# Optimization experiments

Hardware: AMD Instinct MI355X
Metric: run time of the kernel (lower is better)

## Reference

```python
import jax, jax.numpy as jnp
import numpy as np

B, T, V, E, H, L = 16, 64, 50257, 512, 1024, 2


def _gru_layer(x, h0, W_ih, W_hh, b_ih, b_hh):
    # x: (T, B, I), h0: (B, H). PyTorch GRU gate order: r, z, n.
    xp = jnp.einsum('tbi,gi->tbg', x, W_ih) + b_ih  # precompute input gates (T, B, 3H)

    def step(h, xt):
        gh = h @ W_hh.T + b_hh
        xr, xz, xn = jnp.split(xt, 3, axis=-1)
        hr, hz, hn = jnp.split(gh, 3, axis=-1)
        r = jax.nn.sigmoid(xr + hr)
        z = jax.nn.sigmoid(xz + hz)
        n = jnp.tanh(xn + r * hn)
        h_new = (1.0 - z) * n + z * h
        return h_new, h_new

    hT, ys = jax.lax.scan(step, h0, xp)
    return ys, hT


def _gru(x, h0, layer_params):
    # h0: (L, B, H); stacked 2-layer GRU (dropout=0)
    hs = []
    for l in range(L):
        x, hl = _gru_layer(x, h0[l], *layer_params[l])
        hs.append(hl)
    return x, jnp.stack(hs)


def setup_inputs() -> dict:
    key = jax.random.key(0)
    ks = jax.random.split(key, 16)
    s = 0.03  # weight init scale
    return {
        'init_input': jax.random.normal(ks[0], (B, E), jnp.float32),
        'helper': jax.random.randint(ks[1], (B, T), 0, V),
        'emb': jax.random.normal(ks[2], (V, E), jnp.float32) * 0.1,
        'W_ih0': jax.random.normal(ks[3], (3 * H, 2 * E), jnp.float32) * s,
        'W_hh0': jax.random.normal(ks[4], (3 * H, H), jnp.float32) * s,
        'b_ih0': jax.random.normal(ks[5], (3 * H,), jnp.float32) * s,
        'b_hh0': jax.random.normal(ks[6], (3 * H,), jnp.float32) * s,
        'W_ih1': jax.random.normal(ks[7], (3 * H, H), jnp.float32) * s,
        'W_hh1': jax.random.normal(ks[8], (3 * H, H), jnp.float32) * s,
        'b_ih1': jax.random.normal(ks[9], (3 * H,), jnp.float32) * s,
        'b_hh1': jax.random.normal(ks[10], (3 * H,), jnp.float32) * s,
        'Wc_w': jax.random.normal(ks[11], (E, H), jnp.float32) * s,
        'Wc_b': jax.random.normal(ks[12], (E,), jnp.float32) * s,
    }


def reference(init_input, helper, emb, W_ih0, W_hh0, b_ih0, b_hh0,
              W_ih1, W_hh1, b_ih1, b_hh1, Wc_w, Wc_b):
    params = [(W_ih0, W_hh0, b_ih0, b_hh0), (W_ih1, W_hh1, b_ih1, b_hh1)]
    # h_0 from one GRU step over cat([init_input, init_input]) with zero state
    x0 = jnp.concatenate([init_input, init_input], axis=-1)[None]  # (1, B, 2E)
    h_zero = jnp.zeros((L, B, H), init_input.dtype)
    _, h0 = _gru(x0, h_zero, params)
    # teacher-forcing decode: helper embeddings concat with cond (init_input)
    helper_emb = emb[helper].transpose(1, 0, 2)  # (T, B, E)
    cond = jnp.broadcast_to(init_input[None], (T, B, E))
    x = jnp.concatenate([helper_emb, cond], axis=-1)  # (T, B, 2E)
    outputs, _ = _gru(x, h0, params)  # (T, B, H)
    final = jnp.tanh(jnp.einsum('tbh,eh->tbe', outputs, Wc_w) + Wc_b)  # (T, B, E)
    # dot-product word-embedding attention -> vocab logits, then transpose(0,1)
    logits = jnp.einsum('tbe,ve->btv', final, emb)  # (B, T, V)
    return logits
```

## Files before the change

### kernel.cpp

```cpp
#include <hip/hip_runtime.h>
#include <math.h>

#define Bc 16
#define Tc 64
#define Vc 50257
#define Ec 512
#define Hc 1024
#define SCAN_BLOCKS 256

typedef __attribute__((ext_vector_type(4))) float f32x4;
typedef __attribute__((ext_vector_type(8))) __bf16 bf16x8;

__device__ __forceinline__ float dot4(float4 a, float4 b) {
    return a.x * b.x + a.y * b.y + a.z * b.z + a.w * b.w;
}
__device__ __forceinline__ float sigm(float x) { return 1.0f / (1.0f + expf(-x)); }

__device__ __forceinline__ unsigned short f2b(float f) {
    unsigned u = __float_as_uint(f);
    unsigned r = u + 0x7fffu + ((u >> 16) & 1u);
    return (unsigned short)(r >> 16);
}
__device__ __forceinline__ float b2f(unsigned short b) {
    return __uint_as_float(((unsigned)b) << 16);
}
__device__ __forceinline__ float2 u2f2(unsigned long long u) {
    union { unsigned long long u; float2 f; } c;
    c.u = u;
    return c.f;
}
__device__ __forceinline__ unsigned long long f22u(float a, float b) {
    union { float f[2]; unsigned long long u; } c;
    c.f[0] = a;
    c.f[1] = b;
    return c.u;
}

__global__ __launch_bounds__(256) void split_bf16_4(const float4* __restrict__ x,
                                                    ushort4* __restrict__ hi,
                                                    ushort4* __restrict__ lo, int n4) {
    int i = blockIdx.x * 256 + threadIdx.x;
    for (; i < n4; i += gridDim.x * 256) {
        float4 v = x[i];
        ushort4 h, l;
        h.x = f2b(v.x); l.x = f2b(v.x - b2f(h.x));
        h.y = f2b(v.y); l.y = f2b(v.y - b2f(h.y));
        h.z = f2b(v.z); l.z = f2b(v.z - b2f(h.z));
        h.w = f2b(v.w); l.w = f2b(v.w - b2f(h.w));
        hi[i] = h;
        lo[i] = l;
    }
}

__global__ __launch_bounds__(256) void build_x0(const float* __restrict__ emb,
                                                const int* __restrict__ helper,
                                                const float* __restrict__ init,
                                                float* __restrict__ X0) {
    int idx = blockIdx.x * 256 + threadIdx.x;
    const int total = Tc * Bc * 1024;
    for (int i = idx; i < total; i += gridDim.x * 256) {
        int m = i >> 10;
        int c = i & 1023;
        int t = m >> 4;
        int b = m & 15;
        float v;
        if (c < 512) {
            int w = helper[b * Tc + t];
            v = emb[(size_t)w * Ec + c];
        } else {
            v = init[b * Ec + (c - 512)];
        }
        X0[i] = v;
    }
}

__global__ __launch_bounds__(256) void h0_layer(const float* __restrict__ xin,
                                                const float* __restrict__ Wih,
                                                const float* __restrict__ bih,
                                                const float* __restrict__ bhh,
                                                float* __restrict__ h0out, int dup) {
    __shared__ float xs[1024];
    int b = blockIdx.x >> 2;
    int hseg = blockIdx.x & 3;
    int tid = threadIdx.x;
    for (int i = tid; i < 1024; i += 256)
        xs[i] = dup ? xin[b * 512 + (i & 511)] : xin[b * 1024 + i];
    __syncthreads();
    int hidx = hseg * 256 + tid;
    const float* wr = Wih + (size_t)hidx * 1024;
    const float* wz = Wih + (size_t)(Hc + hidx) * 1024;
    const float* wn = Wih + (size_t)(2 * Hc + hidx) * 1024;
    float ar = 0.f, az = 0.f, an = 0.f;
    for (int k = 0; k < 1024; k += 4) {
        float4 x4 = *(const float4*)&xs[k];
        ar += dot4(*(const float4*)&wr[k], x4);
        az += dot4(*(const float4*)&wz[k], x4);
        an += dot4(*(const float4*)&wn[k], x4);
    }
    float r = sigm(ar + bih[hidx] + bhh[hidx]);
    float z = sigm(az + bih[Hc + hidx] + bhh[Hc + hidx]);
    float n = tanhf(an + bih[2 * Hc + hidx] + r * bhh[2 * Hc + hidx]);
    h0out[b * Hc + hidx] = (1.f - z) * n;
}

__global__ __launch_bounds__(512) void gru_scan(const float* __restrict__ xp,
                                                const float* __restrict__ Whh,
                                                const float* __restrict__ bhh,
                                                float* __restrict__ ys,
                                                unsigned* __restrict__ bar) {
    extern __shared__ char lds_pad[];
    __shared__ float wlds[12][1024];
    int tid = threadIdx.x;
    int g0 = blockIdx.x * 4;

    for (int i = tid; i < 12 * 256; i += 512) {
        int r = i >> 8, c = i & 255;
        int hl = r / 3, gate = r % 3;
        ((float4*)wlds[r])[c] =
            ((const float4*)&Whh[(size_t)(gate * Hc + g0 + hl) * Hc])[c];
    }

    int b = tid >> 5;
    int kseg = tid & 31;

    float bh[12];
    float hold[4];
    if (kseg == 0) {
#pragma unroll
        for (int r = 0; r < 12; ++r) {
            int hl = r / 3, gate = r % 3;
            bh[r] = bhh[gate * Hc + g0 + hl];
        }
        float4 h4 = *(const float4*)&ys[b * Hc + g0];
        hold[0] = h4.x; hold[1] = h4.y; hold[2] = h4.z; hold[3] = h4.w;
    }
    __syncthreads();

    unsigned* leaf = bar + (blockIdx.x & 15) * 32;
    unsigned* root = bar + 512;

    for (int t = 0; t < Tc; ++t) {
        float xg[3][4];
        if (kseg == 0) {
            const float* xrow = xp + (size_t)(t * Bc + b) * 3072 + g0;
#pragma unroll
            for (int gte = 0; gte < 3; ++gte) {
                float4 v = *(const float4*)&xrow[gte * 1024];
                xg[gte][0] = v.x; xg[gte][1] = v.y; xg[gte][2] = v.z; xg[gte][3] = v.w;
            }
        }
        const unsigned long long* hsrc =
            (const unsigned long long*)(ys + (size_t)t * (Bc * Hc)) + b * 512 + kseg;
        float2 hv[16];
#pragma unroll
        for (int q = 0; q < 16; ++q)
            hv[q] = u2f2(__hip_atomic_load(hsrc + q * 32, __ATOMIC_RELAXED,
                                           __HIP_MEMORY_SCOPE_AGENT));
        float acc[12];
#pragma unroll
        for (int r = 0; r < 12; ++r) {
            const float2* w = (const float2*)&wlds[r][kseg * 2];
            float s = 0.f;
#pragma unroll
            for (int q = 0; q < 16; ++q) {
                float2 ww = w[q * 32];
                s += ww.x * hv[q].x + ww.y * hv[q].y;
            }
            acc[r] = s;
        }
#pragma unroll
        for (int r = 0; r < 12; ++r) {
            float s = acc[r];
            s += __shfl_xor(s, 1);
            s += __shfl_xor(s, 2);
            s += __shfl_xor(s, 4);
            s += __shfl_xor(s, 8);
            s += __shfl_xor(s, 16);
            acc[r] = s;
        }
        if (kseg == 0) {
            float hnew[4];
#pragma unroll
            for (int hl = 0; hl < 4; ++hl) {
                float r_ = sigm(xg[0][hl] + acc[hl * 3 + 0] + bh[hl * 3 + 0]);
                float z_ = sigm(xg[1][hl] + acc[hl * 3 + 1] + bh[hl * 3 + 1]);
                float n_ = tanhf(xg[2][hl] + r_ * (acc[hl * 3 + 2] + bh[hl * 3 + 2]));
                hnew[hl] = (1.f - z_) * n_ + z_ * hold[hl];
                hold[hl] = hnew[hl];
            }
            unsigned long long* dst =
                (unsigned long long*)(ys + (size_t)(t + 1) * (Bc * Hc) + b * Hc + g0);
            __hip_atomic_store(dst, f22u(hnew[0], hnew[1]), __ATOMIC_RELAXED,
                               __HIP_MEMORY_SCOPE_AGENT);
            __hip_atomic_store(dst + 1, f22u(hnew[2], hnew[3]), __ATOMIC_RELAXED,
                               __HIP_MEMORY_SCOPE_AGENT);
        }
        if (t < Tc - 1) {
            __syncthreads();
            if (tid == 0) {
                unsigned old = __hip_atomic_fetch_add(leaf, 1u, __ATOMIC_RELAXED,
                                                      __HIP_MEMORY_SCOPE_AGENT);
                if (old == (unsigned)(t * 16 + 15))
                    __hip_atomic_fetch_add(root, 1u, __ATOMIC_RELAXED,
                                           __HIP_MEMORY_SCOPE_AGENT);
                unsigned tgt = (unsigned)((t + 1) * 16);
                while (__hip_atomic_load(root, __ATOMIC_RELAXED,
                                         __HIP_MEMORY_SCOPE_AGENT) < tgt)
                    __builtin_amdgcn_s_sleep(1);
            }
            __syncthreads();
        }
    }
}

#define GLD_LDS16(g, l)                                                        \
    __builtin_amdgcn_global_load_lds(                                          \
        (const __attribute__((address_space(1))) unsigned int*)(g),            \
        (__attribute__((address_space(3))) unsigned int*)(l), 16, 0, 0)

__global__ __launch_bounds__(256) void mfma_gemm_split(
    const unsigned short* __restrict__ Ah, const unsigned short* __restrict__ Al,
    const unsigned short* __restrict__ Bh, const unsigned short* __restrict__ Bl,
    const float* __restrict__ bias, float* __restrict__ C, int N, int K, int ldc,
    int act, int remap) {
    __shared__ __align__(16) unsigned short As[128 * 32];
    __shared__ __align__(16) unsigned short Bs[128 * 32];
    int tid = threadIdx.x;
    int m0 = blockIdx.y * 128, n0 = blockIdx.x * 128;
    int wave = tid >> 6, lane = tid & 63;
    int mh = (wave >> 1) * 64, nh = (wave & 1) * 64;
    int rlane = lane & 15, k8 = (lane >> 4) * 8;

    f32x4 zero = {0.f, 0.f, 0.f, 0.f};
    f32x4 acc[4][4];
#pragma unroll
    for (int i = 0; i < 4; ++i)
#pragma unroll
        for (int j = 0; j < 4; ++j) acc[i][j] = zero;

    const unsigned short* Ap[3] = {Ah, Al, Ah};
    const unsigned short* Bp[3] = {Bh, Bh, Bl};

    int c0 = tid, c1 = tid + 256;
    int ar0 = m0 + (c0 >> 2), ak0 = (c0 & 3) * 8;
    int ar1 = m0 + (c1 >> 2), ak1 = (c1 & 3) * 8;
    int br0 = n0 + (c0 >> 2);
    int br1 = n0 + (c1 >> 2);
    if (br0 >= N) br0 = N - 1;
    if (br1 >= N) br1 = N - 1;

    for (int ph = 0; ph < 3; ++ph) {
        const unsigned short* Ab = Ap[ph];
        const unsigned short* Bb = Bp[ph];
        for (int kt = 0; kt < K; kt += 32) {
            GLD_LDS16(&Ab[(size_t)ar0 * K + kt + ak0], &As[c0 * 8]);
            GLD_LDS16(&Ab[(size_t)ar1 * K + kt + ak1], &As[c1 * 8]);
            GLD_LDS16(&Bb[(size_t)br0 * K + kt + ak0], &Bs[c0 * 8]);
            GLD_LDS16(&Bb[(size_t)br1 * K + kt + ak1], &Bs[c1 * 8]);
            __syncthreads();
            bf16x8 a[4], b[4];
#pragma unroll
            for (int f = 0; f < 4; ++f)
                a[f] = *(const bf16x8*)&As[(mh + f * 16 + rlane) * 32 + k8];
#pragma unroll
            for (int f = 0; f < 4; ++f)
                b[f] = *(const bf16x8*)&Bs[(nh + f * 16 + rlane) * 32 + k8];
#pragma unroll
            for (int mf = 0; mf < 4; ++mf)
#pragma unroll
                for (int nf = 0; nf < 4; ++nf)
                    acc[mf][nf] = __builtin_amdgcn_mfma_f32_16x16x32_bf16(
                        a[mf], b[nf], acc[mf][nf], 0, 0, 0);
            __syncthreads();
        }
    }

    int quad = lane >> 4;
#pragma unroll
    for (int nf = 0; nf < 4; ++nf) {
        int n = n0 + nh + nf * 16 + rlane;
        if (n >= N) continue;
        float bv = bias ? bias[n] : 0.f;
#pragma unroll
        for (int mf = 0; mf < 4; ++mf) {
#pragma unroll
            for (int r = 0; r < 4; ++r) {
                int m = m0 + mh + mf * 16 + quad * 4 + r;
                float x = acc[mf][nf][r] + bv;
                if (act) x = tanhf(x);
                int orow = remap ? ((m & 15) * Tc + (m >> 4)) : m;
                C[(size_t)orow * ldc + n] = x;
            }
        }
    }
}

extern "C" void kernel_launch(void* const* d_in, const int* in_sizes, int n_in,
                              void* d_out, int out_size, void* d_ws, size_t ws_size,
                              hipStream_t stream) {
    const float* init   = (const float*)d_in[0];
    const int*   helper = (const int*)d_in[1];
    const float* emb    = (const float*)d_in[2];
    const float* W_ih0  = (const float*)d_in[3];
    const float* W_hh0  = (const float*)d_in[4];
    const float* b_ih0  = (const float*)d_in[5];
    const float* b_hh0  = (const float*)d_in[6];
    const float* W_ih1  = (const float*)d_in[7];
    const float* W_hh1  = (const float*)d_in[8];
    const float* b_ih1  = (const float*)d_in[9];
    const float* b_hh1  = (const float*)d_in[10];
    const float* Wc_w   = (const float*)d_in[11];
    const float* Wc_b   = (const float*)d_in[12];
    float* out = (float*)d_out;

    const int embN = Vc * Ec;

    char* p = (char*)d_ws;
    auto alloc = [&](size_t bytes) {
        char* r = p;
        p += (bytes + 255) & ~(size_t)255;
        return r;
    };
    float* X0   = (float*)alloc((size_t)1048576 * 4);
    float* xp0  = (float*)alloc((size_t)3145728 * 4);
    float* xp1  = (float*)alloc((size_t)3145728 * 4);
    float* ys0x = (float*)alloc((size_t)65 * 16384 * 4);
    float* ys1x = (float*)alloc((size_t)65 * 16384 * 4);
    float* fin  = (float*)alloc((size_t)524288 * 4);
    unsigned* bar = (unsigned*)alloc(8192);
    unsigned short* embh = (unsigned short*)alloc((size_t)embN * 2);
    unsigned short* embl = (unsigned short*)alloc((size_t)embN * 2);
    unsigned short* X0h  = (unsigned short*)alloc((size_t)1048576 * 2);
    unsigned short* X0l  = (unsigned short*)alloc((size_t)1048576 * 2);
    unsigned short* Wi0h = (unsigned short*)alloc((size_t)3145728 * 2);
    unsigned short* Wi0l = (unsigned short*)alloc((size_t)3145728 * 2);
    unsigned short* Wi1h = (unsigned short*)alloc((size_t)3145728 * 2);
    unsigned short* Wi1l = (unsigned short*)alloc((size_t)3145728 * 2);
    unsigned short* Wch  = (unsigned short*)alloc((size_t)524288 * 2);
    unsigned short* Wcl  = (unsigned short*)alloc((size_t)524288 * 2);
    unsigned short* ys0h = (unsigned short*)alloc((size_t)1048576 * 2);
    unsigned short* ys0l = (unsigned short*)alloc((size_t)1048576 * 2);
    unsigned short* ys1h = (unsigned short*)alloc((size_t)1048576 * 2);
    unsigned short* ys1l = (unsigned short*)alloc((size_t)1048576 * 2);
    unsigned short* finh = (unsigned short*)alloc((size_t)524288 * 2);
    unsigned short* finl = (unsigned short*)alloc((size_t)524288 * 2);

    hipMemsetAsync(bar, 0, 8192, stream);

    auto split = [&](const float* src, unsigned short* h, unsigned short* l, int n) {
        int n4 = n / 4;
        int grid = (n4 + 255) / 256;
        if (grid > 4096) grid = 4096;
        split_bf16_4<<<grid, 256, 0, stream>>>((const float4*)src, (ushort4*)h,
                                               (ushort4*)l, n4);
    };

    split(emb, embh, embl, embN);
    split(W_ih0, Wi0h, Wi0l, 3145728);
    split(W_ih1, Wi1h, Wi1l, 3145728);
    split(Wc_w, Wch, Wcl, 524288);

    h0_layer<<<64, 256, 0, stream>>>(init, W_ih0, b_ih0, b_hh0, ys0x, 1);
    h0_layer<<<64, 256, 0, stream>>>(ys0x, W_ih1, b_ih1, b_hh1, ys1x, 0);

    build_x0<<<1024, 256, 0, stream>>>(emb, helper, init, X0);
    split(X0, X0h, X0l, 1048576);
    mfma_gemm_split<<<dim3(24, 8), 256, 0, stream>>>(X0h, X0l, Wi0h, Wi0l, b_ih0,
                                                     xp0, 3072, 1024, 3072, 0, 0);
    gru_scan<<<SCAN_BLOCKS, 512, 40960, stream>>>(xp0, W_hh0, b_hh0, ys0x, bar);

    split(ys0x + 16384, ys0h, ys0l, 1048576);
    mfma_gemm_split<<<dim3(24, 8), 256, 0, stream>>>(ys0h, ys0l, Wi1h, Wi1l, b_ih1,
                                                     xp1, 3072, 1024, 3072, 0, 0);
    gru_scan<<<SCAN_BLOCKS, 512, 40960, stream>>>(xp1, W_hh1, b_hh1, ys1x, bar + 1024);

    split(ys1x + 16384, ys1h, ys1l, 1048576);
    mfma_gemm_split<<<dim3(4, 8), 256, 0, stream>>>(ys1h, ys1l, Wch, Wcl, Wc_b,
                                                    fin, 512, 1024, 512, 1, 0);

    split(fin, finh, finl, 524288);
    mfma_gemm_split<<<dim3((Vc + 127) / 128, 8), 256, 0, stream>>>(
        finh, finl, embh, embl, nullptr, out, Vc, 512, Vc, 0, 1);
}
```

Baseline: 2.258 ms.

## Wavefront-pipeline both GRU layers in one persistent scan kernel

Merges the two per-layer GRU scan kernels into one persistent kernel that runs layer 1 one step behind layer 0 (a wavefront over t=0..T). Layer 1's input projection is computed inside the scan from LDS-resident W_ih1 instead of a separate split + MFMA GEMM. This removes one kernel launch, one grid-wide barrier sequence of 64 steps, and the intermediate GEMM and split. The cost is 48K extra LDS plus a heavier per-step fp32 dot-product load per block, and W_ih1 is now applied in plain fp32 rather than through the split-bf16 MFMA path.

```diff
diff --git a/kernel.cpp b/kernel.cpp
--- a/kernel.cpp
+++ b/kernel.cpp
@@ -103,99 +103,195 @@
     h0out[b * Hc + hidx] = (1.f - z) * n;
 }
 
-__global__ __launch_bounds__(512) void gru_scan(const float* __restrict__ xp,
-                                                const float* __restrict__ Whh,
-                                                const float* __restrict__ bhh,
-                                                float* __restrict__ ys,
-                                                unsigned* __restrict__ bar) {
-    extern __shared__ char lds_pad[];
-    __shared__ float wlds[12][1024];
+__global__ __launch_bounds__(512) void gru_scan2(
+    const float* __restrict__ xp0, const float* __restrict__ Whh0,
+    const float* __restrict__ bhh0, const float* __restrict__ Wih1,
+    const float* __restrict__ Whh1, const float* __restrict__ bih1,
+    const float* __restrict__ bhh1, float* __restrict__ ys0,
+    float* __restrict__ ys1, unsigned* __restrict__ bar) {
+    extern __shared__ float wdyn[];
+    __shared__ float wh0[12][1024];
+    float* wi1 = wdyn;
+    float* wh1 = wdyn + 12 * 1024;
     int tid = threadIdx.x;
     int g0 = blockIdx.x * 4;
 
     for (int i = tid; i < 12 * 256; i += 512) {
         int r = i >> 8, c = i & 255;
         int hl = r / 3, gate = r % 3;
-        ((float4*)wlds[r])[c] =
-            ((const float4*)&Whh[(size_t)(gate * Hc + g0 + hl) * Hc])[c];
+        size_t row = (size_t)(gate * Hc + g0 + hl) * Hc;
+        ((float4*)wh0[r])[c] = ((const float4*)&Whh0[row])[c];
+        ((float4*)&wi1[r * 1024])[c] = ((const float4*)&Wih1[row])[c];
+        ((float4*)&wh1[r * 1024])[c] = ((const float4*)&Whh1[row])[c];
     }
 
     int b = tid >> 5;
     int kseg = tid & 31;
 
-    float bh[12];
-    float hold[4];
+    float bh0[12], brz1[8], bnx1[4], bnh1[4];
+    float hold0[4], hold1[4];
     if (kseg == 0) {
 #pragma unroll
         for (int r = 0; r < 12; ++r) {
             int hl = r / 3, gate = r % 3;
-            bh[r] = bhh[gate * Hc + g0 + hl];
-        }
-        float4 h4 = *(const float4*)&ys[b * Hc + g0];
-        hold[0] = h4.x; hold[1] = h4.y; hold[2] = h4.z; hold[3] = h4.w;
+            bh0[r] = bhh0[gate * Hc + g0 + hl];
+        }
+#pragma unroll
+        for (int hl = 0; hl < 4; ++hl) {
+            brz1[hl * 2 + 0] = bih1[g0 + hl] + bhh1[g0 + hl];
+            brz1[hl * 2 + 1] = bih1[Hc + g0 + hl] + bhh1[Hc + g0 + hl];
+            bnx1[hl] = bih1[2 * Hc + g0 + hl];
+            bnh1[hl] = bhh1[2 * Hc + g0 + hl];
+        }
+        float4 h4 = *(const float4*)&ys0[b * Hc + g0];
+        hold0[0] = h4.x; hold0[1] = h4.y; hold0[2] = h4.z; hold0[3] = h4.w;
+        float4 h5 = *(const float4*)&ys1[b * Hc + g0];
+        hold1[0] = h5.x; hold1[1] = h5.y; hold1[2] = h5.z; hold1[3] = h5.w;
     }
     __syncthreads();
 
     unsigned* leaf = bar + (blockIdx.x & 15) * 32;
     unsigned* root = bar + 512;
 
-    for (int t = 0; t < Tc; ++t) {
+    for (int t = 0; t <= Tc; ++t) {
+        const bool doL0 = (t < Tc);
+        const bool doL1 = (t > 0);
+
         float xg[3][4];
+        if (doL0 && kseg == 0) {
+            const float* xrow = xp0 + (size_t)(t * Bc + b) * 3072 + g0;
+#pragma unroll
+            for (int g = 0; g < 3; ++g) {
+                float4 v = *(const float4*)&xrow[g * 1024];
+                xg[g][0] = v.x; xg[g][1] = v.y; xg[g][2] = v.z; xg[g][3] = v.w;
+            }
+        }
+
+        const unsigned long long* h0src =
+            (const unsigned long long*)(ys0 + (size_t)t * (Bc * Hc)) + b * 512 + kseg;
+        float2 hv0[16];
+#pragma unroll
+        for (int q = 0; q < 16; ++q)
+            hv0[q] = u2f2(__hip_atomic_load(h0src + q * 32, __ATOMIC_RELAXED,
+                                            __HIP_MEMORY_SCOPE_AGENT));
+        float2 hv1[16];
+        if (doL1) {
+            const unsigned long long* h1src =
+                (const unsigned long long*)(ys1 + (size_t)(t - 1) * (Bc * Hc)) +
+                b * 512 + kseg;
+#pragma unroll
+            for (int q = 0; q < 16; ++q)
+                hv1[q] = u2f2(__hip_atomic_load(h1src + q * 32, __ATOMIC_RELAXED,
+                                                __HIP_MEMORY_SCOPE_AGENT));
+        }
+
+        float acc0[12];
+        if (doL0) {
+#pragma unroll
+            for (int r = 0; r < 12; ++r) {
+                const float2* w = (const float2*)&wh0[r][kseg * 2];
+                float s = 0.f;
+#pragma unroll
+                for (int q = 0; q < 16; ++q) {
+                    float2 ww = w[q * 32];
+                    s += ww.x * hv0[q].x + ww.y * hv0[q].y;
+                }
+                acc0[r] = s;
+            }
+        }
+
+        float a1[16];
+        if (doL1) {
+#pragma unroll
+            for (int hl = 0; hl < 4; ++hl) {
+#pragma unroll
+                for (int gate = 0; gate < 3; ++gate) {
+                    int r = hl * 3 + gate;
+                    const float2* wx = (const float2*)&wi1[r * 1024 + kseg * 2];
+                    const float2* wh = (const float2*)&wh1[r * 1024 + kseg * 2];
+                    float sx = 0.f, sh = 0.f;
+#pragma unroll
+                    for (int q = 0; q < 16; ++q) {
+                        float2 wwx = wx[q * 32];
+                        sx += wwx.x * hv0[q].x + wwx.y * hv0[q].y;
+                        float2 wwh = wh[q * 32];
+                        sh += wwh.x * hv1[q].x + wwh.y * hv1[q].y;
+                    }
+                    if (gate < 2)
+                        a1[hl * 4 + gate] = sx + sh;
+                    else {
+                        a1[hl * 4 + 2] = sx;
+                        a1[hl * 4 + 3] = sh;
+                    }
+                }
+            }
+        }
+
+        if (doL0) {
+#pragma unroll
+            for (int r = 0; r < 12; ++r) {
+                float s = acc0[r];
+                s += __shfl_xor(s, 1);
+                s += __shfl_xor(s, 2);
+                s += __shfl_xor(s, 4);
+                s += __shfl_xor(s, 8);
+                s += __shfl_xor(s, 16);
+                acc0[r] = s;
+            }
+        }
+        if (doL1) {
+#pragma unroll
+            for (int i = 0; i < 16; ++i) {
+                float s = a1[i];
+                s += __shfl_xor(s, 1);
+                s += __shfl_xor(s, 2);
+                s += __shfl_xor(s, 4);
+                s += __shfl_xor(s, 8);
+                s += __shfl_xor(s, 16);
+                a1[i] = s;
+            }
+        }
+
         if (kseg == 0) {
-            const float* xrow = xp + (size_t)(t * Bc + b) * 3072 + g0;
-#pragma unroll
-            for (int gte = 0; gte < 3; ++gte) {
-                float4 v = *(const float4*)&xrow[gte * 1024];
-                xg[gte][0] = v.x; xg[gte][1] = v.y; xg[gte][2] = v.z; xg[gte][3] = v.w;
-            }
-        }
-        const unsigned long long* hsrc =
-            (const unsigned long long*)(ys + (size_t)t * (Bc * Hc)) + b * 512 + kseg;
-        float2 hv[16];
-#pragma unroll
-        for (int q = 0; q < 16; ++q)
-            hv[q] = u2f2(__hip_atomic_load(hsrc + q * 32, __ATOMIC_RELAXED,
-                                           __HIP_MEMORY_SCOPE_AGENT));
-        float acc[12];
-#pragma unroll
-        for (int r = 0; r < 12; ++r) {
-            const float2* w = (const float2*)&wlds[r][kseg * 2];
-            float s = 0.f;
-#pragma unroll
-            for (int q = 0; q < 16; ++q) {
-                float2 ww = w[q * 32];
-                s += ww.x * hv[q].x + ww.y * hv[q].y;
-            }
-            acc[r] = s;
-        }
-#pragma unroll
-        for (int r = 0; r < 12; ++r) {
-            float s = acc[r];
-            s += __shfl_xor(s, 1);
-            s += __shfl_xor(s, 2);
-            s += __shfl_xor(s, 4);
-            s += __shfl_xor(s, 8);
-            s += __shfl_xor(s, 16);
-            acc[r] = s;
-        }
-        if (kseg == 0) {
-            float hnew[4];
-#pragma unroll
-            for (int hl = 0; hl < 4; ++hl) {
-                float r_ = sigm(xg[0][hl] + acc[hl * 3 + 0] + bh[hl * 3 + 0]);
-                float z_ = sigm(xg[1][hl] + acc[hl * 3 + 1] + bh[hl * 3 + 1]);
-                float n_ = tanhf(xg[2][hl] + r_ * (acc[hl * 3 + 2] + bh[hl * 3 + 2]));
-                hnew[hl] = (1.f - z_) * n_ + z_ * hold[hl];
-                hold[hl] = hnew[hl];
-            }
-            unsigned long long* dst =
-                (unsigned long long*)(ys + (size_t)(t + 1) * (Bc * Hc) + b * Hc + g0);
-            __hip_atomic_store(dst, f22u(hnew[0], hnew[1]), __ATOMIC_RELAXED,
-                               __HIP_MEMORY_SCOPE_AGENT);
-            __hip_atomic_store(dst + 1, f22u(hnew[2], hnew[3]), __ATOMIC_RELAXED,
-                               __HIP_MEMORY_SCOPE_AGENT);
-        }
-        if (t < Tc - 1) {
+            if (doL0) {
+                float hnew[4];
+#pragma unroll
+                for (int hl = 0; hl < 4; ++hl) {
+                    float r_ = sigm(xg[0][hl] + acc0[hl * 3 + 0] + bh0[hl * 3 + 0]);
+                    float z_ = sigm(xg[1][hl] + acc0[hl * 3 + 1] + bh0[hl * 3 + 1]);
+                    float n_ =
+                        tanhf(xg[2][hl] + r_ * (acc0[hl * 3 + 2] + bh0[hl * 3 + 2]));
+                    hnew[hl] = (1.f - z_) * n_ + z_ * hold0[hl];
+                    hold0[hl] = hnew[hl];
+                }
+                unsigned long long* dst = (unsigned long long*)(ys0 +
+                    (size_t)(t + 1) * (Bc * Hc) + b * Hc + g0);
+                __hip_atomic_store(dst, f22u(hnew[0], hnew[1]), __ATOMIC_RELAXED,
+                                   __HIP_MEMORY_SCOPE_AGENT);
+                __hip_atomic_store(dst + 1, f22u(hnew[2], hnew[3]), __ATOMIC_RELAXED,
+                                   __HIP_MEMORY_SCOPE_AGENT);
+            }
+            if (doL1) {
+                float hnew[4];
+#pragma unroll
+                for (int hl = 0; hl < 4; ++hl) {
+                    float r_ = sigm(a1[hl * 4 + 0] + brz1[hl * 2 + 0]);
+                    float z_ = sigm(a1[hl * 4 + 1] + brz1[hl * 2 + 1]);
+                    float n_ = tanhf(a1[hl * 4 + 2] + bnx1[hl] +
+                                     r_ * (a1[hl * 4 + 3] + bnh1[hl]));
+                    hnew[hl] = (1.f - z_) * n_ + z_ * hold1[hl];
+                    hold1[hl] = hnew[hl];
+                }
+                unsigned long long* dst = (unsigned long long*)(ys1 +
+                    (size_t)t * (Bc * Hc) + b * Hc + g0);
+                __hip_atomic_store(dst, f22u(hnew[0], hnew[1]), __ATOMIC_RELAXED,
+                                   __HIP_MEMORY_SCOPE_AGENT);
+                __hip_atomic_store(dst + 1, f22u(hnew[2], hnew[3]), __ATOMIC_RELAXED,
+                                   __HIP_MEMORY_SCOPE_AGENT);
+            }
+        }
+
+        if (t < Tc) {
             __syncthreads();
             if (tid == 0) {
                 unsigned old = __hip_atomic_fetch_add(leaf, 1u, __ATOMIC_RELAXED,
@@ -323,7 +419,6 @@
     };
     float* X0   = (float*)alloc((size_t)1048576 * 4);
     float* xp0  = (float*)alloc((size_t)3145728 * 4);
-    float* xp1  = (float*)alloc((size_t)3145728 * 4);
     float* ys0x = (float*)alloc((size_t)65 * 16384 * 4);
     float* ys1x = (float*)alloc((size_t)65 * 16384 * 4);
     float* fin  = (float*)alloc((size_t)524288 * 4);
@@ -334,12 +429,8 @@
     unsigned short* X0l  = (unsigned short*)alloc((size_t)1048576 * 2);
     unsigned short* Wi0h = (unsigned short*)alloc((size_t)3145728 * 2);
     unsigned short* Wi0l = (unsigned short*)alloc((size_t)3145728 * 2);
-    unsigned short* Wi1h = (unsigned short*)alloc((size_t)3145728 * 2);
-    unsigned short* Wi1l = (unsigned short*)alloc((size_t)3145728 * 2);
     unsigned short* Wch  = (unsigned short*)alloc((size_t)524288 * 2);
     unsigned short* Wcl  = (unsigned short*)alloc((size_t)524288 * 2);
-    unsigned short* ys0h = (unsigned short*)alloc((size_t)1048576 * 2);
-    unsigned short* ys0l = (unsigned short*)alloc((size_t)1048576 * 2);
     unsigned short* ys1h = (unsigned short*)alloc((size_t)1048576 * 2);
     unsigned short* ys1l = (unsigned short*)alloc((size_t)1048576 * 2);
     unsigned short* finh = (unsigned short*)alloc((size_t)524288 * 2);
@@ -357,7 +448,6 @@
 
     split(emb, embh, embl, embN);
     split(W_ih0, Wi0h, Wi0l, 3145728);
-    split(W_ih1, Wi1h, Wi1l, 3145728);
     split(Wc_w, Wch, Wcl, 524288);
 
     h0_layer<<<64, 256, 0, stream>>>(init, W_ih0, b_ih0, b_hh0, ys0x, 1);
@@ -367,12 +457,9 @@
     split(X0, X0h, X0l, 1048576);
     mfma_gemm_split<<<dim3(24, 8), 256, 0, stream>>>(X0h, X0l, Wi0h, Wi0l, b_ih0,
                                                      xp0, 3072, 1024, 3072, 0, 0);
-    gru_scan<<<SCAN_BLOCKS, 512, 40960, stream>>>(xp0, W_hh0, b_hh0, ys0x, bar);
-
-    split(ys0x + 16384, ys0h, ys0l, 1048576);
-    mfma_gemm_split<<<dim3(24, 8), 256, 0, stream>>>(ys0h, ys0l, Wi1h, Wi1l, b_ih1,
-                                                     xp1, 3072, 1024, 3072, 0, 0);
-    gru_scan<<<SCAN_BLOCKS, 512, 40960, stream>>>(xp1, W_hh1, b_hh1, ys1x, bar + 1024);
+
+    gru_scan2<<<SCAN_BLOCKS, 512, 24 * 1024 * 4, stream>>>(
+        xp0, W_hh0, b_hh0, W_ih1, W_hh1, b_ih1, b_hh1, ys0x, ys1x, bar);
 
     split(ys1x + 16384, ys1h, ys1l, 1048576);
     mfma_gemm_split<<<dim3(4, 8), 256, 0, stream>>>(ys1h, ys1l, Wch, Wcl, Wc_b,
```

After: 2.385 ms. 5.6% more time.

## Rewrite GRU recurrent scan with split-bf16 MFMA and single-wave blocks

Applied to the files above, without the earlier changes.

Replaces the FP32 scalar-dot recurrent scan with a 64-thread-per-block kernel that computes h@W_hh using bf16 hi/lo split MFMA (four products per k-tile), with W_hh converted to swizzled bf16 halves in LDS. The hidden state is now stored directly as bf16 hi/lo pairs, so the separate split kernels before the next-layer GEMMs are dropped. The grid barrier is simplified to a single-wave spin without __syncthreads. It trades more per-step global loads of the hi/lo state and a small LDS transpose for less per-step FP32 arithmetic and shuffle reductions; precision now rests on the three-term bf16 split.

```diff
diff --git a/kernel.cpp b/kernel.cpp
--- a/kernel.cpp
+++ b/kernel.cpp
@@ -23,17 +23,6 @@
 }
 __device__ __forceinline__ float b2f(unsigned short b) {
     return __uint_as_float(((unsigned)b) << 16);
-}
-__device__ __forceinline__ float2 u2f2(unsigned long long u) {
-    union { unsigned long long u; float2 f; } c;
-    c.u = u;
-    return c.f;
-}
-__device__ __forceinline__ unsigned long long f22u(float a, float b) {
-    union { float f[2]; unsigned long long u; } c;
-    c.f[0] = a;
-    c.f[1] = b;
-    return c.u;
 }
 
 __global__ __launch_bounds__(256) void split_bf16_4(const float4* __restrict__ x,
@@ -78,7 +67,10 @@
                                                 const float* __restrict__ Wih,
                                                 const float* __restrict__ bih,
                                                 const float* __restrict__ bhh,
-                                                float* __restrict__ h0out, int dup) {
+                                                float* __restrict__ h0out,
+                                                unsigned short* __restrict__ ysh,
+                                                unsigned short* __restrict__ ysl,
+                                                int dup) {
     __shared__ float xs[1024];
     int b = blockIdx.x >> 2;
     int hseg = blockIdx.x & 3;
@@ -100,115 +92,158 @@
     float r = sigm(ar + bih[hidx] + bhh[hidx]);
     float z = sigm(az + bih[Hc + hidx] + bhh[Hc + hidx]);
     float n = tanhf(an + bih[2 * Hc + hidx] + r * bhh[2 * Hc + hidx]);
-    h0out[b * Hc + hidx] = (1.f - z) * n;
-}
-
-__global__ __launch_bounds__(512) void gru_scan(const float* __restrict__ xp,
-                                                const float* __restrict__ Whh,
-                                                const float* __restrict__ bhh,
-                                                float* __restrict__ ys,
-                                                unsigned* __restrict__ bar) {
-    extern __shared__ char lds_pad[];
-    __shared__ float wlds[12][1024];
-    int tid = threadIdx.x;
-    int g0 = blockIdx.x * 4;
-
-    for (int i = tid; i < 12 * 256; i += 512) {
+    float h = (1.f - z) * n;
+    h0out[b * Hc + hidx] = h;
+    unsigned short hb = f2b(h);
+    ysh[b * 1024 + hidx] = hb;
+    ysl[b * 1024 + hidx] = f2b(h - b2f(hb));
+}
+
+__global__ __launch_bounds__(64, 1) void gru_scan_mfma(
+    const float* __restrict__ xp, const float* __restrict__ Whh,
+    const float* __restrict__ bhh, unsigned short* __restrict__ ysh,
+    unsigned short* __restrict__ ysl, unsigned* __restrict__ bar) {
+    extern __shared__ unsigned short Wlo[];
+    __shared__ unsigned short Whi[16][1024];
+    __shared__ float dxc[16][16];
+    const int lane = threadIdx.x;
+    const int g0 = blockIdx.x * 4;
+    const int brow = lane & 15;
+    const int kq = lane >> 4;
+
+    for (int i = lane; i < 12 * 256; i += 64) {
         int r = i >> 8, c = i & 255;
-        int hl = r / 3, gate = r % 3;
-        ((float4*)wlds[r])[c] =
-            ((const float4*)&Whh[(size_t)(gate * Hc + g0 + hl) * Hc])[c];
-    }
-
-    int b = tid >> 5;
-    int kseg = tid & 31;
+        size_t wrow = (size_t)((r >> 2) * Hc + g0 + (r & 3)) * Hc;
+        float4 w4 = *(const float4*)&Whh[wrow + c * 4];
+        ushort4 h4, l4;
+        h4.x = f2b(w4.x); l4.x = f2b(w4.x - b2f(h4.x));
+        h4.y = f2b(w4.y); l4.y = f2b(w4.y - b2f(h4.y));
+        h4.z = f2b(w4.z); l4.z = f2b(w4.z - b2f(h4.z));
+        h4.w = f2b(w4.w); l4.w = f2b(w4.w - b2f(h4.w));
+        int bo = (c * 8) ^ ((r & 7) << 4);
+        *(ushort4*)((char*)&Whi[r][0] + bo) = h4;
+        *(ushort4*)((char*)&Wlo[r * 1024] + bo) = l4;
+    }
+    ushort4 z4 = {0, 0, 0, 0};
+    for (int i = lane; i < 4 * 256; i += 64) {
+        int r = 12 + (i >> 8), c = i & 255;
+        ((ushort4*)&Whi[r][0])[c] = z4;
+        ((ushort4*)&Wlo[r * 1024])[c] = z4;
+    }
 
     float bh[12];
+#pragma unroll
+    for (int r = 0; r < 12; ++r) bh[r] = bhh[(r >> 2) * Hc + g0 + (r & 3)];
+
     float hold[4];
-    if (kseg == 0) {
-#pragma unroll
-        for (int r = 0; r < 12; ++r) {
-            int hl = r / 3, gate = r % 3;
-            bh[r] = bhh[gate * Hc + g0 + hl];
-        }
-        float4 h4 = *(const float4*)&ys[b * Hc + g0];
-        hold[0] = h4.x; hold[1] = h4.y; hold[2] = h4.z; hold[3] = h4.w;
+    {
+        const unsigned long long* s0h =
+            (const unsigned long long*)ysh + (size_t)brow * 256 + blockIdx.x;
+        const unsigned long long* s0l =
+            (const unsigned long long*)ysl + (size_t)brow * 256 + blockIdx.x;
+        union { unsigned long long u; ushort4 s; } ch, cl;
+        ch.u = __hip_atomic_load(s0h, __ATOMIC_RELAXED, __HIP_MEMORY_SCOPE_AGENT);
+        cl.u = __hip_atomic_load(s0l, __ATOMIC_RELAXED, __HIP_MEMORY_SCOPE_AGENT);
+        hold[0] = b2f(ch.s.x) + b2f(cl.s.x);
+        hold[1] = b2f(ch.s.y) + b2f(cl.s.y);
+        hold[2] = b2f(ch.s.z) + b2f(cl.s.z);
+        hold[3] = b2f(ch.s.w) + b2f(cl.s.w);
     }
     __syncthreads();
+
+    const char* wha = (const char*)&Whi[0][0] + brow * 2048;
+    const char* wla = (const char*)Wlo + brow * 2048;
+    const int swz = (brow & 7) << 4;
 
     unsigned* leaf = bar + (blockIdx.x & 15) * 32;
     unsigned* root = bar + 512;
 
     for (int t = 0; t < Tc; ++t) {
-        float xg[3][4];
-        if (kseg == 0) {
-            const float* xrow = xp + (size_t)(t * Bc + b) * 3072 + g0;
-#pragma unroll
-            for (int gte = 0; gte < 3; ++gte) {
-                float4 v = *(const float4*)&xrow[gte * 1024];
-                xg[gte][0] = v.x; xg[gte][1] = v.y; xg[gte][2] = v.z; xg[gte][3] = v.w;
+        const unsigned long long* bsh =
+            (const unsigned long long*)ysh + (size_t)(t * 16 + brow) * 256 + kq * 2;
+        const unsigned long long* bsl =
+            (const unsigned long long*)ysl + (size_t)(t * 16 + brow) * 256 + kq * 2;
+        unsigned long long vh[64], vl[64];
+#pragma unroll
+        for (int kt = 0; kt < 32; ++kt) {
+            vh[kt * 2] = __hip_atomic_load(bsh + kt * 8, __ATOMIC_RELAXED,
+                                           __HIP_MEMORY_SCOPE_AGENT);
+            vh[kt * 2 + 1] = __hip_atomic_load(bsh + kt * 8 + 1, __ATOMIC_RELAXED,
+                                               __HIP_MEMORY_SCOPE_AGENT);
+            vl[kt * 2] = __hip_atomic_load(bsl + kt * 8, __ATOMIC_RELAXED,
+                                           __HIP_MEMORY_SCOPE_AGENT);
+            vl[kt * 2 + 1] = __hip_atomic_load(bsl + kt * 8 + 1, __ATOMIC_RELAXED,
+                                               __HIP_MEMORY_SCOPE_AGENT);
+        }
+        const float* xrow = xp + (size_t)(t * 16 + brow) * 3072 + g0;
+        f32x4 xgr = *(const f32x4*)&xrow[0];
+        f32x4 xgz = *(const f32x4*)&xrow[1024];
+        f32x4 xgn = *(const f32x4*)&xrow[2048];
+
+        f32x4 zz = {0.f, 0.f, 0.f, 0.f};
+        f32x4 acc[4];
+        acc[0] = zz; acc[1] = zz; acc[2] = zz; acc[3] = zz;
+#pragma unroll
+        for (int kt = 0; kt < 32; ++kt) {
+            bf16x8 ah = *(const bf16x8*)(wha + ((kt * 64 + kq * 16) ^ swz));
+            bf16x8 al = *(const bf16x8*)(wla + ((kt * 64 + kq * 16) ^ swz));
+            union { unsigned long long u[2]; bf16x8 v; } ch, cl;
+            ch.u[0] = vh[kt * 2]; ch.u[1] = vh[kt * 2 + 1];
+            cl.u[0] = vl[kt * 2]; cl.u[1] = vl[kt * 2 + 1];
+            acc[kt & 3] = __builtin_amdgcn_mfma_f32_16x16x32_bf16(ah, ch.v,
+                                                                  acc[kt & 3], 0, 0, 0);
+            acc[kt & 3] = __builtin_amdgcn_mfma_f32_16x16x32_bf16(ah, cl.v,
+                                                                  acc[kt & 3], 0, 0, 0);
+            acc[kt & 3] = __builtin_amdgcn_mfma_f32_16x16x32_bf16(al, ch.v,
+                                                                  acc[kt & 3], 0, 0, 0);
+            acc[kt & 3] = __builtin_amdgcn_mfma_f32_16x16x32_bf16(al, cl.v,
+                                                                  acc[kt & 3], 0, 0, 0);
+        }
+        f32x4 d = acc[0] + acc[1] + acc[2] + acc[3];
+        if (kq < 3) *(f32x4*)&dxc[brow][kq * 4] = d;
+        __syncthreads();
+
+        if (lane < 16) {
+            f32x4 ghr = *(const f32x4*)&dxc[lane][0];
+            f32x4 ghz = *(const f32x4*)&dxc[lane][4];
+            f32x4 ghn = *(const f32x4*)&dxc[lane][8];
+            union { unsigned long long u; ushort4 s; } ph, pl;
+            float hn4[4];
+#pragma unroll
+            for (int hl = 0; hl < 4; ++hl) {
+                float r_ = sigm(xgr[hl] + ghr[hl] + bh[hl]);
+                float z_ = sigm(xgz[hl] + ghz[hl] + bh[4 + hl]);
+                float n_ = tanhf(xgn[hl] + r_ * (ghn[hl] + bh[8 + hl]));
+                float h = (1.f - z_) * n_ + z_ * hold[hl];
+                hold[hl] = h;
+                hn4[hl] = h;
             }
-        }
-        const unsigned long long* hsrc =
-            (const unsigned long long*)(ys + (size_t)t * (Bc * Hc)) + b * 512 + kseg;
-        float2 hv[16];
-#pragma unroll
-        for (int q = 0; q < 16; ++q)
-            hv[q] = u2f2(__hip_atomic_load(hsrc + q * 32, __ATOMIC_RELAXED,
-                                           __HIP_MEMORY_SCOPE_AGENT));
-        float acc[12];
-#pragma unroll
-        for (int r = 0; r < 12; ++r) {
-            const float2* w = (const float2*)&wlds[r][kseg * 2];
-            float s = 0.f;
-#pragma unroll
-            for (int q = 0; q < 16; ++q) {
-                float2 ww = w[q * 32];
-                s += ww.x * hv[q].x + ww.y * hv[q].y;
-            }
-            acc[r] = s;
-        }
-#pragma unroll
-        for (int r = 0; r < 12; ++r) {
-            float s = acc[r];
-            s += __shfl_xor(s, 1);
-            s += __shfl_xor(s, 2);
-            s += __shfl_xor(s, 4);
-            s += __shfl_xor(s, 8);
-            s += __shfl_xor(s, 16);
-            acc[r] = s;
-        }
-        if (kseg == 0) {
-            float hnew[4];
-#pragma unroll
-            for (int hl = 0; hl < 4; ++hl) {
-                float r_ = sigm(xg[0][hl] + acc[hl * 3 + 0] + bh[hl * 3 + 0]);
-                float z_ = sigm(xg[1][hl] + acc[hl * 3 + 1] + bh[hl * 3 + 1]);
-                float n_ = tanhf(xg[2][hl] + r_ * (acc[hl * 3 + 2] + bh[hl * 3 + 2]));
-                hnew[hl] = (1.f - z_) * n_ + z_ * hold[hl];
-                hold[hl] = hnew[hl];
-            }
-            unsigned long long* dst =
-                (unsigned long long*)(ys + (size_t)(t + 1) * (Bc * Hc) + b * Hc + g0);
-            __hip_atomic_store(dst, f22u(hnew[0], hnew[1]), __ATOMIC_RELAXED,
-                               __HIP_MEMORY_SCOPE_AGENT);
-            __hip_atomic_store(dst + 1, f22u(hnew[2], hnew[3]), __ATOMIC_RELAXED,
-                               __HIP_MEMORY_SCOPE_AGENT);
-        }
+            ph.s.x = f2b(hn4[0]); pl.s.x = f2b(hn4[0] - b2f(ph.s.x));
+            ph.s.y = f2b(hn4[1]); pl.s.y = f2b(hn4[1] - b2f(ph.s.y));
+            ph.s.z = f2b(hn4[2]); pl.s.z = f2b(hn4[2] - b2f(ph.s.z));
+            ph.s.w = f2b(hn4[3]); pl.s.w = f2b(hn4[3] - b2f(ph.s.w));
+            unsigned long long* dh = (unsigned long long*)ysh +
+                                     (size_t)((t + 1) * 16 + lane) * 256 + blockIdx.x;
+            unsigned long long* dl = (unsigned long long*)ysl +
+                                     (size_t)((t + 1) * 16 + lane) * 256 + blockIdx.x;
+            __hip_atomic_store(dh, ph.u, __ATOMIC_RELAXED, __HIP_MEMORY_SCOPE_AGENT);
+            __hip_atomic_store(dl, pl.u, __ATOMIC_RELAXED, __HIP_MEMORY_SCOPE_AGENT);
+        }
+
         if (t < Tc - 1) {
-            __syncthreads();
-            if (tid == 0) {
+            asm volatile("s_waitcnt vmcnt(0)" ::: "memory");
+            if (lane == 0) {
                 unsigned old = __hip_atomic_fetch_add(leaf, 1u, __ATOMIC_RELAXED,
                                                       __HIP_MEMORY_SCOPE_AGENT);
                 if (old == (unsigned)(t * 16 + 15))
                     __hip_atomic_fetch_add(root, 1u, __ATOMIC_RELAXED,
                                            __HIP_MEMORY_SCOPE_AGENT);
-                unsigned tgt = (unsigned)((t + 1) * 16);
-                while (__hip_atomic_load(root, __ATOMIC_RELAXED,
-                                         __HIP_MEMORY_SCOPE_AGENT) < tgt)
-                    __builtin_amdgcn_s_sleep(1);
             }
-            __syncthreads();
+            unsigned tgt = (unsigned)((t + 1) * 16);
+            while (__hip_atomic_load(root, __ATOMIC_RELAXED,
+                                     __HIP_MEMORY_SCOPE_AGENT) < tgt)
+                __builtin_amdgcn_s_sleep(1);
+            asm volatile("" ::: "memory");
         }
     }
 }
@@ -314,6 +349,7 @@
     float* out = (float*)d_out;
 
     const int embN = Vc * Ec;
+    const size_t ysN = (size_t)65 * 16 * 1024;
 
     char* p = (char*)d_ws;
     auto alloc = [&](size_t bytes) {
@@ -324,9 +360,9 @@
     float* X0   = (float*)alloc((size_t)1048576 * 4);
     float* xp0  = (float*)alloc((size_t)3145728 * 4);
     float* xp1  = (float*)alloc((size_t)3145728 * 4);
-    float* ys0x = (float*)alloc((size_t)65 * 16384 * 4);
-    float* ys1x = (float*)alloc((size_t)65 * 16384 * 4);
     float* fin  = (float*)alloc((size_t)524288 * 4);
+    float* h00  = (float*)alloc((size_t)16384 * 4);
+    float* h01  = (float*)alloc((size_t)16384 * 4);
     unsigned* bar = (unsigned*)alloc(8192);
     unsigned short* embh = (unsigned short*)alloc((size_t)embN * 2);
     unsigned short* embl = (unsigned short*)alloc((size_t)embN * 2);
@@ -338,10 +374,10 @@
     unsigned short* Wi1l = (unsigned short*)alloc((size_t)3145728 * 2);
     unsigned short* Wch  = (unsigned short*)alloc((size_t)524288 * 2);
     unsigned short* Wcl  = (unsigned short*)alloc((size_t)524288 * 2);
-    unsigned short* ys0h = (unsigned short*)alloc((size_t)1048576 * 2);
-    unsigned short* ys0l = (unsigned short*)alloc((size_t)1048576 * 2);
-    unsigned short* ys1h = (unsigned short*)alloc((size_t)1048576 * 2);
-    unsigned short* ys1l = (unsigned short*)alloc((size_t)1048576 * 2);
+    unsigned short* ys0h = (unsigned short*)alloc(ysN * 2);
+    unsigned short* ys0l = (unsigned short*)alloc(ysN * 2);
+    unsigned short* ys1h = (unsigned short*)alloc(ysN * 2);
+    unsigned short* ys1l = (unsigned short*)alloc(ysN * 2);
     unsigned short* finh = (unsigned short*)alloc((size_t)524288 * 2);
     unsigned short* finl = (unsigned short*)alloc((size_t)524288 * 2);
 
@@ -360,23 +396,27 @@
     split(W_ih1, Wi1h, Wi1l, 3145728);
     split(Wc_w, Wch, Wcl, 524288);
 
-    h0_layer<<<64, 256, 0, stream>>>(init, W_ih0, b_ih0, b_hh0, ys0x, 1);
-    h0_layer<<<64, 256, 0, stream>>>(ys0x, W_ih1, b_ih1, b_hh1, ys1x, 0);
+    h0_layer<<<64, 256, 0, stream>>>(init, W_ih0, b_ih0, b_hh0, h00, ys0h, ys0l, 1);
+    h0_layer<<<64, 256, 0, stream>>>(h00, W_ih1, b_ih1, b_hh1, h01, ys1h, ys1l, 0);
 
     build_x0<<<1024, 256, 0, stream>>>(emb, helper, init, X0);
     split(X0, X0h, X0l, 1048576);
     mfma_gemm_split<<<dim3(24, 8), 256, 0, stream>>>(X0h, X0l, Wi0h, Wi0l, b_ih0,
                                                      xp0, 3072, 1024, 3072, 0, 0);
-    gru_scan<<<SCAN_BLOCKS, 512, 40960, stream>>>(xp0, W_hh0, b_hh0, ys0x, bar);
-
-    split(ys0x + 16384, ys0h, ys0l, 1048576);
-    mfma_gemm_split<<<dim3(24, 8), 256, 0, stream>>>(ys0h, ys0l, Wi1h, Wi1l, b_ih1,
-                                                     xp1, 3072, 1024, 3072, 0, 0);
-    gru_scan<<<SCAN_BLOCKS, 512, 40960, stream>>>(xp1, W_hh1, b_hh1, ys1x, bar + 1024);
-
-    split(ys1x + 16384, ys1h, ys1l, 1048576);
-    mfma_gemm_split<<<dim3(4, 8), 256, 0, stream>>>(ys1h, ys1l, Wch, Wcl, Wc_b,
-                                                    fin, 512, 1024, 512, 1, 0);
+
+    gru_scan_mfma<<<SCAN_BLOCKS, 64, 32768, stream>>>(xp0, W_hh0, b_hh0, ys0h, ys0l,
+                                                      bar);
+
+    mfma_gemm_split<<<dim3(24, 8), 256, 0, stream>>>(ys0h + 16384, ys0l + 16384,
+                                                     Wi1h, Wi1l, b_ih1, xp1, 3072,
+                                                     1024, 3072, 0, 0);
+
+    gru_scan_mfma<<<SCAN_BLOCKS, 64, 32768, stream>>>(xp1, W_hh1, b_hh1, ys1h, ys1l,
+                                                      bar + 1024);
+
+    mfma_gemm_split<<<dim3(4, 8), 256, 0, stream>>>(ys1h + 16384, ys1l + 16384,
+                                                    Wch, Wcl, Wc_b, fin, 512, 1024,
+                                                    512, 1, 0);
 
     split(fin, finh, finl, 524288);
     mfma_gemm_split<<<dim3((Vc + 127) / 128, 8), 256, 0, stream>>>(
```

Measured after the change: 2.273 ms. About the same (+0.6%).
